# Kernel tuning notes

Hardware: AMD Instinct MI355X
Metric: run time of the kernel (lower is better)

The kernel has to match this reference:

```python
import jax, jax.numpy as jnp
import numpy as np

K = 16  # number of neighbors (init kwarg k)
N_POINTS = 8_000_000
D_FEAT = 6


def setup_inputs() -> dict:
    key = jax.random.key(0)
    k1, k2, k3 = jax.random.split(key, 3)
    P = jax.random.normal(k1, (N_POINTS, D_FEAT), dtype=jnp.float32)
    W = jax.random.normal(k2, (3, 10), dtype=jnp.float32) * 0.1  # nn.Linear(10, 3) weight
    b = jax.random.normal(k3, (3,), dtype=jnp.float32) * 0.1     # nn.Linear(10, 3) bias
    i = 12345
    return {"P": P, "W": W, "b": b, "i": i}


def reference(P, W, b, i):
    # --- knn(i): note torch .topk defaults to largest=True, so this faithfully
    # selects the K points with the LARGEST distance to point i.
    pi = P[i, :3]                                   # [3]
    d = jnp.linalg.norm(P[:, :3] - pi, axis=1)      # [N] streaming distance pass
    _, idx = jax.lax.top_k(d, K)                    # [K]
    near = P[idx]                                   # [K, D]
    nloc = near[:, :3]                              # [K, 3]

    # --- rel_pos_enc, vectorized over all K neighbors (one tiny GEMM)
    diff = pi[None, :] - nloc                       # [K, 3]
    dist = jnp.linalg.norm(diff, axis=1, keepdims=True)  # [K, 1]
    feat = jnp.concatenate(
        [jnp.broadcast_to(pi, (K, 3)), nloc, diff, dist], axis=1
    )                                               # [K, 10]
    R = feat @ W.T + b                              # [K, 3]

    # --- forward: concat neighbor coords with encoding
    return jnp.concatenate([nloc, R], axis=1)       # [K, 6]
```

## Files before the change

kernel.cpp:

```cpp
#include <hip/hip_runtime.h>
#include <math.h>

#define KTOP 16
#define B1   504
#define T1   512
#define NC   (B1 * KTOP)
#define T2   512

typedef unsigned long long ull;

__device__ __forceinline__ ull pack_key(float d, unsigned idx) {
    return ((ull)__float_as_uint(d) << 32) | (ull)(0xFFFFFFFFu - idx);
}

__device__ __forceinline__ void insert_key(ull (&k)[KTOP], ull key) {
    ull t = key;
#pragma unroll
    for (int j = 0; j < KTOP; ++j) {
        const ull a = k[j];
        const bool c = (t > a);
        k[j] = c ? t : a;
        t    = c ? a : t;
    }
}

__device__ __forceinline__ float dist3(float x, float y, float z,
                                       float px, float py, float pz) {
#pragma clang fp contract(off)
    const float dx = x - px;
    const float dy = y - py;
    const float dz = z - pz;
    const float s  = (dx * dx + dy * dy) + dz * dz;
    return sqrtf(s);
}

__global__ __launch_bounds__(T1, 1) void pass1_topk(const float* __restrict__ P,
                                                    const int*   __restrict__ ipq,
                                                    int n,
                                                    ull* __restrict__ cand) {
    const int tid    = threadIdx.x;
    const int gid    = blockIdx.x * T1 + tid;
    const int stride = B1 * T1;

    const int i0 = ipq[0];
    const float pix = P[6 * i0 + 0];
    const float piy = P[6 * i0 + 1];
    const float piz = P[6 * i0 + 2];

    ull k[KTOP];
#pragma unroll
    for (int j = 0; j < KTOP; ++j) k[j] = 0ull;

    const float4* __restrict__ P4 = (const float4*)P;
    const int nPairs = n >> 1;

    for (int pp = gid; pp < nPairs; pp += stride) {
        const float4 q0 = P4[3 * pp + 0];
        const float4 q1 = P4[3 * pp + 1];
        const float4 q2 = P4[3 * pp + 2];
        const float dA = dist3(q0.x, q0.y, q0.z, pix, piy, piz);
        const float dB = dist3(q1.z, q1.w, q2.x, pix, piy, piz);
        const ull keyA = pack_key(dA, (unsigned)(2 * pp));
        const ull keyB = pack_key(dB, (unsigned)(2 * pp + 1));
        if (keyA > k[KTOP - 1]) insert_key(k, keyA);
        if (keyB > k[KTOP - 1]) insert_key(k, keyB);
    }
    if ((n & 1) && gid == 0) {
        const int p = n - 1;
        const float d = dist3(P[6 * p], P[6 * p + 1], P[6 * p + 2], pix, piy, piz);
        const ull key = pack_key(d, (unsigned)p);
        if (key > k[KTOP - 1]) insert_key(k, key);
    }

    __shared__ ull s_w[T1 / 64];
    __shared__ ull s_best;
    const int lane = tid & 63;
    const int wid  = tid >> 6;

    for (int r = 0; r < KTOP; ++r) {
        const ull mk = k[0];
        ull rv = mk;
#pragma unroll
        for (int m = 32; m >= 1; m >>= 1) {
            const ull ov = __shfl_xor(rv, m);
            if (ov > rv) rv = ov;
        }
        if (lane == 0) s_w[wid] = rv;
        __syncthreads();
        if (tid == 0) {
            ull b = s_w[0];
            for (int w = 1; w < T1 / 64; ++w) if (s_w[w] > b) b = s_w[w];
            s_best = b;
            cand[blockIdx.x * KTOP + r] = b;
        }
        __syncthreads();
        if (mk == s_best) {
#pragma unroll
            for (int j = 0; j < KTOP - 1; ++j) k[j] = k[j + 1];
            k[KTOP - 1] = 0ull;
        }
    }
}

__global__ __launch_bounds__(T2, 1) void pass2_final(const float* __restrict__ P,
                                                     const int*   __restrict__ ipq,
                                                     const float* __restrict__ W,
                                                     const float* __restrict__ bvec,
                                                     const ull*   __restrict__ cand,
                                                     float* __restrict__ out) {
    __shared__ ull keys[NC];
    __shared__ ull s_w[T2 / 64];
    __shared__ ull s_best;
    __shared__ ull s_final[KTOP];

    const int tid  = threadIdx.x;
    const int lane = tid & 63;
    const int wid  = tid >> 6;

    ull mk = 0ull; int ms = -1;
#pragma unroll
    for (int j = 0; j < 16; ++j) {
        const int s = tid + j * T2;
        if (s < NC) {
            const ull v = cand[s];
            keys[s] = v;
            if (v > mk) { mk = v; ms = s; }
        }
    }
    __syncthreads();

    for (int r = 0; r < KTOP; ++r) {
        ull rv = mk;
#pragma unroll
        for (int m = 32; m >= 1; m >>= 1) {
            const ull ov = __shfl_xor(rv, m);
            if (ov > rv) rv = ov;
        }
        if (lane == 0) s_w[wid] = rv;
        __syncthreads();
        if (tid == 0) {
            ull b = s_w[0];
            for (int w = 1; w < T2 / 64; ++w) if (s_w[w] > b) b = s_w[w];
            s_best = b;
            s_final[r] = b;
        }
        __syncthreads();
        const ull best = s_best;
        if (mk == best) {
            keys[ms] = 0ull;
            mk = 0ull; ms = -1;
#pragma unroll
            for (int j = 0; j < 16; ++j) {
                const int s = tid + j * T2;
                if (s < NC) {
                    const ull v = keys[s];
                    if (v > mk) { mk = v; ms = s; }
                }
            }
        }
    }
    __syncthreads();

    if (tid < KTOP) {
        const ull kk = s_final[tid];
        const float d = __uint_as_float((unsigned)(kk >> 32));
        const unsigned idx = 0xFFFFFFFFu - (unsigned)(kk & 0xFFFFFFFFull);
        const int   i0  = ipq[0];
        const float pix = P[6 * i0 + 0], piy = P[6 * i0 + 1], piz = P[6 * i0 + 2];
        const float nx  = P[6 * (size_t)idx + 0];
        const float ny  = P[6 * (size_t)idx + 1];
        const float nz  = P[6 * (size_t)idx + 2];
        float dx, dy, dz;
        {
#pragma clang fp contract(off)
            dx = pix - nx; dy = piy - ny; dz = piz - nz;
        }
        const float feat[10] = { pix, piy, piz, nx, ny, nz, dx, dy, dz, d };
        float R[3];
#pragma unroll
        for (int r = 0; r < 3; ++r) {
            float acc = bvec[r];
#pragma unroll
            for (int c = 0; c < 10; ++c) acc += feat[c] * W[r * 10 + c];
            R[r] = acc;
        }
        out[6 * tid + 0] = nx;   out[6 * tid + 1] = ny;   out[6 * tid + 2] = nz;
        out[6 * tid + 3] = R[0]; out[6 * tid + 4] = R[1]; out[6 * tid + 5] = R[2];
    }
}

extern "C" void kernel_launch(void* const* d_in, const int* in_sizes, int n_in,
                              void* d_out, int out_size, void* d_ws, size_t ws_size,
                              hipStream_t stream) {
    const float* P    = (const float*)d_in[0];
    const float* W    = (const float*)d_in[1];
    const float* bvec = (const float*)d_in[2];
    const int*   ipq  = (const int*)d_in[3];
    float*       out  = (float*)d_out;

    const int n = in_sizes[0] / 6;
    ull* cand = (ull*)d_ws;

    pass1_topk<<<B1, T1, 0, stream>>>(P, ipq, n, cand);
    pass2_final<<<1, T2, 0, stream>>>(P, ipq, W, bvec, cand, out);
}
```

Baseline: 293.1 us.

## Replace barrier-heavy block top-k merges with wave-level merges and nontemporal loads

Pass 1 now has each wavefront extract its own top-16 with shuffles, with no block barriers per round. The results go to shared memory and wave 0 merges the 8x16 candidates, which replaces 32 block-wide syncs per block. Pass 2 becomes a single wavefront that streams the candidates into per-lane sorted registers and merges them with shuffles instead of repeated shared-memory rescans. The main streaming loop also uses nontemporal vector loads and unroll 2; a single 64-thread pass-2 block trades parallelism for no synchronisation.

```diff
diff --git a/kernel.cpp b/kernel.cpp
--- a/kernel.cpp
+++ b/kernel.cpp
@@ -5,9 +5,10 @@
 #define B1   504
 #define T1   512
 #define NC   (B1 * KTOP)
-#define T2   512
+#define T2   64
 
 typedef unsigned long long ull;
+typedef float f32x4 __attribute__((ext_vector_type(4)));
 
 __device__ __forceinline__ ull pack_key(float d, unsigned idx) {
     return ((ull)__float_as_uint(d) << 32) | (ull)(0xFFFFFFFFu - idx);
@@ -22,6 +23,15 @@
         k[j] = c ? t : a;
         t    = c ? a : t;
     }
+}
+
+__device__ __forceinline__ ull wave_max64(ull v) {
+#pragma unroll
+    for (int m = 32; m >= 1; m >>= 1) {
+        const ull o = __shfl_xor(v, m);
+        if (o > v) v = o;
+    }
+    return v;
 }
 
 __device__ __forceinline__ float dist3(float x, float y, float z,
@@ -51,13 +61,14 @@
 #pragma unroll
     for (int j = 0; j < KTOP; ++j) k[j] = 0ull;
 
-    const float4* __restrict__ P4 = (const float4*)P;
+    const f32x4* __restrict__ P4 = (const f32x4*)P;
     const int nPairs = n >> 1;
 
+#pragma unroll 2
     for (int pp = gid; pp < nPairs; pp += stride) {
-        const float4 q0 = P4[3 * pp + 0];
-        const float4 q1 = P4[3 * pp + 1];
-        const float4 q2 = P4[3 * pp + 2];
+        const f32x4 q0 = __builtin_nontemporal_load(&P4[3 * pp + 0]);
+        const f32x4 q1 = __builtin_nontemporal_load(&P4[3 * pp + 1]);
+        const f32x4 q2 = __builtin_nontemporal_load(&P4[3 * pp + 2]);
         const float dA = dist3(q0.x, q0.y, q0.z, pix, piy, piz);
         const float dB = dist3(q1.z, q1.w, q2.x, pix, piy, piz);
         const ull keyA = pack_key(dA, (unsigned)(2 * pp));
@@ -72,32 +83,30 @@
         if (key > k[KTOP - 1]) insert_key(k, key);
     }
 
-    __shared__ ull s_w[T1 / 64];
-    __shared__ ull s_best;
+    __shared__ ull s_wave[(T1 / 64) * KTOP];
     const int lane = tid & 63;
     const int wid  = tid >> 6;
 
     for (int r = 0; r < KTOP; ++r) {
-        const ull mk = k[0];
-        ull rv = mk;
-#pragma unroll
-        for (int m = 32; m >= 1; m >>= 1) {
-            const ull ov = __shfl_xor(rv, m);
-            if (ov > rv) rv = ov;
-        }
-        if (lane == 0) s_w[wid] = rv;
-        __syncthreads();
-        if (tid == 0) {
-            ull b = s_w[0];
-            for (int w = 1; w < T1 / 64; ++w) if (s_w[w] > b) b = s_w[w];
-            s_best = b;
-            cand[blockIdx.x * KTOP + r] = b;
-        }
-        __syncthreads();
-        if (mk == s_best) {
+        const ull c  = k[0];
+        const ull rv = wave_max64(c);
+        if (lane == 0) s_wave[wid * KTOP + r] = rv;
+        if (c == rv) {
 #pragma unroll
             for (int j = 0; j < KTOP - 1; ++j) k[j] = k[j + 1];
             k[KTOP - 1] = 0ull;
+        }
+    }
+    __syncthreads();
+
+    if (wid == 0) {
+        ull a = s_wave[lane];
+        ull b = s_wave[64 + lane];
+        if (b > a) { const ull t = a; a = b; b = t; }
+        for (int r = 0; r < KTOP; ++r) {
+            const ull rv = wave_max64(a);
+            if (lane == 0) cand[blockIdx.x * KTOP + r] = rv;
+            if (a == rv) { a = b; b = 0ull; }
         }
     }
 }
@@ -108,61 +117,34 @@
                                                      const float* __restrict__ bvec,
                                                      const ull*   __restrict__ cand,
                                                      float* __restrict__ out) {
-    __shared__ ull keys[NC];
-    __shared__ ull s_w[T2 / 64];
-    __shared__ ull s_best;
-    __shared__ ull s_final[KTOP];
+    const int lane = threadIdx.x;
 
-    const int tid  = threadIdx.x;
-    const int lane = tid & 63;
-    const int wid  = tid >> 6;
+    ull k[KTOP];
+#pragma unroll
+    for (int j = 0; j < KTOP; ++j) k[j] = 0ull;
 
-    ull mk = 0ull; int ms = -1;
+    const ulonglong2* __restrict__ c2 = (const ulonglong2*)cand;
+#pragma unroll 2
+    for (int j = lane; j < NC / 2; j += T2) {
+        const ulonglong2 v = c2[j];
+        if (v.x > k[KTOP - 1]) insert_key(k, v.x);
+        if (v.y > k[KTOP - 1]) insert_key(k, v.y);
+    }
+
+    ull mine = 0ull;
+    for (int r = 0; r < KTOP; ++r) {
+        const ull c  = k[0];
+        const ull rv = wave_max64(c);
+        if (lane == r) mine = rv;
+        if (c == rv) {
 #pragma unroll
-    for (int j = 0; j < 16; ++j) {
-        const int s = tid + j * T2;
-        if (s < NC) {
-            const ull v = cand[s];
-            keys[s] = v;
-            if (v > mk) { mk = v; ms = s; }
+            for (int j = 0; j < KTOP - 1; ++j) k[j] = k[j + 1];
+            k[KTOP - 1] = 0ull;
         }
     }
-    __syncthreads();
 
-    for (int r = 0; r < KTOP; ++r) {
-        ull rv = mk;
-#pragma unroll
-        for (int m = 32; m >= 1; m >>= 1) {
-            const ull ov = __shfl_xor(rv, m);
-            if (ov > rv) rv = ov;
-        }
-        if (lane == 0) s_w[wid] = rv;
-        __syncthreads();
-        if (tid == 0) {
-            ull b = s_w[0];
-            for (int w = 1; w < T2 / 64; ++w) if (s_w[w] > b) b = s_w[w];
-            s_best = b;
-            s_final[r] = b;
-        }
-        __syncthreads();
-        const ull best = s_best;
-        if (mk == best) {
-            keys[ms] = 0ull;
-            mk = 0ull; ms = -1;
-#pragma unroll
-            for (int j = 0; j < 16; ++j) {
-                const int s = tid + j * T2;
-                if (s < NC) {
-                    const ull v = keys[s];
-                    if (v > mk) { mk = v; ms = s; }
-                }
-            }
-        }
-    }
-    __syncthreads();
-
-    if (tid < KTOP) {
-        const ull kk = s_final[tid];
+    if (lane < KTOP) {
+        const ull kk = mine;
         const float d = __uint_as_float((unsigned)(kk >> 32));
         const unsigned idx = 0xFFFFFFFFu - (unsigned)(kk & 0xFFFFFFFFull);
         const int   i0  = ipq[0];
@@ -184,8 +166,8 @@
             for (int c = 0; c < 10; ++c) acc += feat[c] * W[r * 10 + c];
             R[r] = acc;
         }
-        out[6 * tid + 0] = nx;   out[6 * tid + 1] = ny;   out[6 * tid + 2] = nz;
-        out[6 * tid + 3] = R[0]; out[6 * tid + 4] = R[1]; out[6 * tid + 5] = R[2];
+        out[6 * lane + 0] = nx;   out[6 * lane + 1] = ny;   out[6 * lane + 2] = nz;
+        out[6 * lane + 3] = R[0]; out[6 * lane + 4] = R[1]; out[6 * lane + 5] = R[2];
     }
 }
 
```

New measurement: 335.6 us. 1.14x slower.
